# Kernel optimization log

Hardware: AMD Instinct MI355X
Metric: run time of the kernel (lower is better)

The kernel has to match this reference:

```python
import jax, jax.numpy as jnp
import numpy as np

N, T, F, T_dim, D = 256, 12, 32, 8, 64

def setup_inputs() -> dict:
    key = jax.random.key(0)
    ks = jax.random.split(key, 8)
    return {
        "x": jax.random.normal(ks[0], (N, T, F), jnp.float32),
        "Wq": jax.random.normal(ks[1], (N * T_dim, F, D), jnp.float32) * 0.1,
        "Wk": jax.random.normal(ks[2], (N * T_dim, F, D), jnp.float32) * 0.1,
        "Wv": jax.random.normal(ks[3], (N * T_dim, F, D), jnp.float32) * 0.1,
        "bq": jnp.zeros((N * T_dim, 1, D), jnp.float32),
        "bk": jnp.zeros((N * T_dim, 1, D), jnp.float32),
        "bv": jnp.zeros((N * T_dim, 1, D), jnp.float32),
        "w1": jax.random.normal(ks[4], (T_dim, T_dim * T * T), jnp.float32) * (2.0 / (T_dim * T * T)) ** 0.5,
        "b1": jnp.zeros((T_dim,), jnp.float32),
        "w2": jax.random.normal(ks[5], (1, T_dim), jnp.float32) * 0.5,
        "b2": jnp.zeros((1,), jnp.float32),
        "w3": jax.random.normal(ks[6], (D, D * T_dim), jnp.float32) * (2.0 / (D * T_dim)) ** 0.5,
        "b3": jnp.zeros((D,), jnp.float32),
        "w4": jax.random.normal(ks[7], (F, D), jnp.float32) * (2.0 / D) ** 0.5,
        "b4": jnp.zeros((F,), jnp.float32),
    }

def reference(x, Wq, Wk, Wv, bq, bk, bv, w1, b1, w2, b2, w3, b3, w4, b4):
    norm = 1.0 / np.sqrt(D).astype(np.float32)
    # mat_a: (N*T_dim, T, F) -- x broadcast across T_dim 'time scales'
    mat_a = jnp.broadcast_to(x[:, None], (N, T_dim, T, F)).reshape(-1, T, F)
    q = jnp.einsum('btf,bfd->btd', mat_a, Wq) + bq  # (N*T_dim, T, D)
    k = jnp.einsum('btf,bfd->btd', mat_a, Wk) + bk
    v = jnp.einsum('btf,bfd->btd', mat_a, Wv) + bv
    q4 = q.reshape(N, T_dim, T, D)
    k4 = k.reshape(N, T_dim, T, D)
    # pairwise scores: (N, N, T_dim, T, T)
    alpha = jnp.einsum('iktd,jksd->ijkts', q4, k4) * norm
    alpha = alpha.reshape(N, N, T_dim * T * T)
    h = jax.nn.relu(alpha @ w1.T + b1)            # (N, N, T_dim); dropout = identity (eval)
    s = (h @ w2.T + b2)[..., 0]                   # (N, N)
    att_score = jax.nn.softmax(s, axis=1)
    v4 = v.reshape(N, T_dim, T, D)
    b = jnp.einsum('ij,jktd->iktd', att_score, v4)   # (N, T_dim, T, D)
    b = b.transpose(0, 2, 3, 1).reshape(N, T, D * T_dim)
    y = jax.nn.relu(b @ w3.T + b3)                # (N, T, D); dropout = identity (eval)
    y = y @ w4.T + b4                             # (N, T, F)
    return (y, att_score)
```

## Files before the change

kernel.cpp:

```cpp
#include <hip/hip_runtime.h>
#include <hip/hip_bf16.h>

typedef unsigned short ushort_t;
typedef __bf16 bf16x8 __attribute__((ext_vector_type(8)));
typedef float f32x4 __attribute__((ext_vector_type(4)));
typedef ushort_t ushort8 __attribute__((ext_vector_type(8)));
typedef ushort_t ushort4v __attribute__((ext_vector_type(4)));

#define GLOAD16(gp, lp) \
    __builtin_amdgcn_global_load_lds((const __attribute__((address_space(1))) void*)(gp), \
                                     (__attribute__((address_space(3))) void*)(lp), 16, 0, 0)

__device__ __forceinline__ ushort_t bf16bits(float x) {
    __hip_bfloat16 h = __float2bfloat16(x);
    return *(ushort_t*)&h;
}
__device__ __forceinline__ float bf2f(ushort_t u) {
    unsigned v = (unsigned)u << 16;
    float f;
    __builtin_memcpy(&f, &v, 4);
    return f;
}

__global__ __launch_bounds__(256) void qkv_kernel(
    const float* __restrict__ x,
    const float* __restrict__ Wq, const float* __restrict__ Wk, const float* __restrict__ Wv,
    const float* __restrict__ bq, const float* __restrict__ bk, const float* __restrict__ bv,
    ushort_t* __restrict__ qhi, ushort_t* __restrict__ kbf, ushort_t* __restrict__ vbf)
{
    __shared__ float xs[4][12 * 36];
    int tid = threadIdx.x;
    int wid = tid >> 6, l = tid & 63;
    int gid = blockIdx.x * 4 + wid;
    int mat = gid >> 11, b = gid & 2047;
    int j = b >> 3;

    const float* W    = (mat == 0) ? Wq : (mat == 1) ? Wk : Wv;
    const float* bias = (mat == 0) ? bq : (mat == 1) ? bk : bv;
    ushort_t*    out  = (mat == 0) ? qhi : (mat == 1) ? kbf : vbf;
    float scale = (mat == 0) ? 0.125f : 1.0f;

    {
        const float4* xsrc = (const float4*)(x + (size_t)j * 384);
        float4 g0 = xsrc[l];
        int flat0 = l * 4;
        float* dst0 = &xs[wid][(flat0 >> 5) * 36 + (flat0 & 31)];
        dst0[0] = g0.x; dst0[1] = g0.y; dst0[2] = g0.z; dst0[3] = g0.w;
        if (l < 32) {
            float4 g1 = xsrc[64 + l];
            int flat1 = 256 + l * 4;
            float* dst1 = &xs[wid][(flat1 >> 5) * 36 + (flat1 & 31)];
            dst1[0] = g1.x; dst1[1] = g1.y; dst1[2] = g1.z; dst1[3] = g1.w;
        }
    }
    __syncthreads();

    int dq = l & 15, tg = l >> 4;
    const f32x4* w4 = (const f32x4*)(W + (size_t)b * 2048);
    f32x4 a0 = {0.f,0.f,0.f,0.f}, a1 = a0, a2 = a0;
    const float* xr = &xs[wid][tg * 3 * 36];
    #pragma unroll
    for (int f4 = 0; f4 < 8; ++f4) {
        f32x4 w0 = w4[(f4 * 4 + 0) * 16 + dq];
        f32x4 w1_ = w4[(f4 * 4 + 1) * 16 + dq];
        f32x4 w2_ = w4[(f4 * 4 + 2) * 16 + dq];
        f32x4 w3_ = w4[(f4 * 4 + 3) * 16 + dq];
        float4 xa = *(const float4*)&xr[0 * 36 + f4 * 4];
        float4 xb = *(const float4*)&xr[1 * 36 + f4 * 4];
        float4 xc = *(const float4*)&xr[2 * 36 + f4 * 4];
        a0 += w0 * xa.x + w1_ * xa.y + w2_ * xa.z + w3_ * xa.w;
        a1 += w0 * xb.x + w1_ * xb.y + w2_ * xb.z + w3_ * xb.w;
        a2 += w0 * xc.x + w1_ * xc.y + w2_ * xc.z + w3_ * xc.w;
    }

    f32x4 bv4 = *(const f32x4*)(bias + (size_t)b * 64 + dq * 4);
    size_t obase = (size_t)b * 768 + dq * 4;
    f32x4 r;
    ushort4v u;
    r = (a0 + bv4) * scale;
    u[0] = bf16bits(r[0]); u[1] = bf16bits(r[1]); u[2] = bf16bits(r[2]); u[3] = bf16bits(r[3]);
    *(ushort4v*)(out + obase + (size_t)(tg * 3 + 0) * 64) = u;
    r = (a1 + bv4) * scale;
    u[0] = bf16bits(r[0]); u[1] = bf16bits(r[1]); u[2] = bf16bits(r[2]); u[3] = bf16bits(r[3]);
    *(ushort4v*)(out + obase + (size_t)(tg * 3 + 1) * 64) = u;
    r = (a2 + bv4) * scale;
    u[0] = bf16bits(r[0]); u[1] = bf16bits(r[1]); u[2] = bf16bits(r[2]); u[3] = bf16bits(r[3]);
    *(ushort4v*)(out + obase + (size_t)(tg * 3 + 2) * 64) = u;
}

__global__ __launch_bounds__(256) void gbuild_kernel(
    const ushort_t* __restrict__ kbf, const float* __restrict__ w1,
    const ushort_t* __restrict__ vbf, const float* __restrict__ w3, const float* __restrict__ w4,
    ushort_t* __restrict__ ghi, ushort_t* __restrict__ vt,
    float* __restrict__ w3t, float* __restrict__ w4t)
{
    __shared__ alignas(16) char sbuf[8448];
    int bx = blockIdx.x, tid = threadIdx.x;

    if (bx < 2048) {
        float* w1s = (float*)sbuf;
        float* ks  = (float*)sbuf + 1152;
        int b = bx, j = b >> 3, kk = b & 7;

        #pragma unroll
        for (int r = 0; r < 2; ++r) {
            int c = r * 256 + tid;
            if (c < 288)
                GLOAD16(w1 + (c / 36) * 1152 + kk * 144 + (c % 36) * 4, &w1s[c * 4]);
        }
        if (tid < 96) {
            ushort8 uu = *(const ushort8*)(kbf + (size_t)b * 768 + tid * 8);
            float4 f0, f1;
            f0.x = bf2f(uu[0]); f0.y = bf2f(uu[1]); f0.z = bf2f(uu[2]); f0.w = bf2f(uu[3]);
            f1.x = bf2f(uu[4]); f1.y = bf2f(uu[5]); f1.z = bf2f(uu[6]); f1.w = bf2f(uu[7]);
            ((float4*)ks)[tid * 2]     = f0;
            ((float4*)ks)[tid * 2 + 1] = f1;
        }
        __syncthreads();

        #pragma unroll
        for (int r = 0; r < 3; ++r) {
            int e = r * 256 + tid;
            int m = e / 96, rem = e - m * 96;
            int t = rem >> 3, d8 = rem & 7;
            const float* w1p = w1s + m * 144 + t * 12;
            float acc[8] = {0.f,0.f,0.f,0.f,0.f,0.f,0.f,0.f};
            #pragma unroll
            for (int s = 0; s < 12; ++s) {
                float wv = w1p[s];
                const float4* kp = (const float4*)(ks + s * 64 + d8 * 8);
                float4 k0 = kp[0], k1 = kp[1];
                acc[0] += wv * k0.x; acc[1] += wv * k0.y;
                acc[2] += wv * k0.z; acc[3] += wv * k0.w;
                acc[4] += wv * k1.x; acc[5] += wv * k1.y;
                acc[6] += wv * k1.z; acc[7] += wv * k1.w;
            }
            ushort8 u;
            #pragma unroll
            for (int dd = 0; dd < 8; ++dd) u[dd] = bf16bits(acc[dd]);
            *(ushort8*)(ghi + ((size_t)j * 8 + m) * 6144 + kk * 768 + t * 64 + d8 * 8) = u;
        }
        return;
    }

    if (bx < 2432) {
        ushort_t (*ts)[264] = (ushort_t(*)[264])sbuf;
        int c0 = (bx - 2048) * 16;
        int cc = tid & 15, jg = tid >> 4;
        #pragma unroll 4
        for (int jj = 0; jj < 16; ++jj) {
            int jx = jg * 16 + jj;
            ts[cc][jx] = vbf[(size_t)jx * 6144 + c0 + cc];
        }
        __syncthreads();
        #pragma unroll
        for (int c = 0; c < 16; ++c)
            vt[(size_t)(c0 + c) * 256 + tid] = ts[c][tid];
        return;
    }
    if (bx < 2448) {
        int wb = bx - 2432;
        #pragma unroll
        for (int r = 0; r < 8; ++r) {
            int e = wb * 2048 + r * 256 + tid;
            int dout = e >> 9, c3 = e & 511;
            int cb = ((c3 & 7) << 6) | (c3 >> 3);
            w3t[cb * 64 + dout] = w3[e];
        }
        return;
    }
    #pragma unroll
    for (int r = 0; r < 8; ++r) {
        int e = r * 256 + tid; int f = e >> 6, dd = e & 63;
        w4t[dd * 32 + f] = w4[e];
    }
}

__global__ __launch_bounds__(256, 2) void hgemm_kernel(
    const ushort_t* __restrict__ qhi, const ushort_t* __restrict__ ghi,
    ushort_t* __restrict__ hpart)
{
    __shared__ ushort_t As[2][128 * 64];
    __shared__ ushort_t Bs[2][128 * 64];

    int tid = threadIdx.x;
    int bid = blockIdx.x;
    int lane = tid & 63, wid = tid >> 6;
    int wr = wid >> 1, wc = wid & 1;
    int xcd = bid & 7, kq = bid >> 3;
    int z = xcd + 8 * (kq >> 5);
    int rem = kq & 31;
    int n0 = (rem & 15) * 128, i0 = (rem >> 4) * 128;
    int kbase = z * 384;
    ushort_t* Hout = hpart + (size_t)z * 524288;

    f32x4 acc[4][4] = {};

    #define STAGE(buf, koff)                                                                 \
    {                                                                                        \
        _Pragma("unroll")                                                                    \
        for (int r = 0; r < 4; ++r) {                                                        \
            int c = r * 256 + tid; int row = c >> 3, slot = c & 7;                           \
            int so = (koff) + ((slot ^ (row & 7)) * 8);                                      \
            GLOAD16(ghi + (size_t)(n0 + row) * 6144 + so, &As[buf][c * 8]);                  \
            GLOAD16(qhi + (size_t)(i0 + row) * 6144 + so, &Bs[buf][c * 8]);                  \
        }                                                                                    \
    }

    STAGE(0, kbase);
    int cur = 0;
    for (int s = 0; s < 6; ++s) {
        __syncthreads();
        if (s + 1 < 6) STAGE(cur ^ 1, kbase + (s + 1) * 64);
        #pragma unroll
        for (int kh = 0; kh < 2; ++kh) {
            bf16x8 a[4], b[4];
            #pragma unroll
            for (int mi = 0; mi < 4; ++mi) {
                int row = wr * 64 + mi * 16 + (lane & 15);
                int slot = (kh * 4 + (lane >> 4)) ^ (row & 7);
                a[mi] = *(const bf16x8*)&As[cur][row * 64 + slot * 8];
            }
            #pragma unroll
            for (int ni = 0; ni < 4; ++ni) {
                int row = wc * 64 + ni * 16 + (lane & 15);
                int slot = (kh * 4 + (lane >> 4)) ^ (row & 7);
                b[ni] = *(const bf16x8*)&Bs[cur][row * 64 + slot * 8];
            }
            #pragma unroll
            for (int mi = 0; mi < 4; ++mi)
                #pragma unroll
                for (int ni = 0; ni < 4; ++ni)
                    acc[mi][ni] = __builtin_amdgcn_mfma_f32_16x16x32_bf16(a[mi], b[ni], acc[mi][ni], 0, 0, 0);
        }
        cur ^= 1;
    }
    #undef STAGE

    int r4 = (lane >> 4) * 4, cn = lane & 15;
    #pragma unroll
    for (int mi = 0; mi < 4; ++mi)
        #pragma unroll
        for (int ni = 0; ni < 4; ++ni) {
            int i = i0 + wc * 64 + ni * 16 + cn;
            int nb = n0 + wr * 64 + mi * 16 + r4;
            ushort4v u;
            #pragma unroll
            for (int r = 0; r < 4; ++r) u[r] = bf16bits(acc[mi][ni][r]);
            *(ushort4v*)(Hout + (size_t)i * 2048 + nb) = u;
        }
}

__global__ __launch_bounds__(256) void score_softmax_kernel(
    const ushort_t* __restrict__ hpart, const float* __restrict__ b1g,
    const float* __restrict__ w2g, const float* __restrict__ b2g,
    float* __restrict__ att, ushort_t* __restrict__ attbf)
{
    int i = blockIdx.x, j = threadIdx.x;
    float hm[8];
    #pragma unroll
    for (int m = 0; m < 8; ++m) hm[m] = b1g[m];
    #pragma unroll 4
    for (int z = 0; z < 16; ++z) {
        ushort8 u = *(const ushort8*)(hpart + (size_t)z * 524288 + (size_t)i * 2048 + j * 8);
        #pragma unroll
        for (int m = 0; m < 8; ++m) hm[m] += bf2f(u[m]);
    }
    float sv = b2g[0];
    #pragma unroll
    for (int m = 0; m < 8; ++m) sv += fmaxf(hm[m], 0.f) * w2g[m];

    __shared__ float wred[4], wred2[4];
    float mx = sv;
    #pragma unroll
    for (int off = 32; off > 0; off >>= 1) mx = fmaxf(mx, __shfl_down(mx, off, 64));
    if ((j & 63) == 0) wred[j >> 6] = mx;
    __syncthreads();
    mx = fmaxf(fmaxf(wred[0], wred[1]), fmaxf(wred[2], wred[3]));

    float e = expf(sv - mx);
    float sum = e;
    #pragma unroll
    for (int off = 32; off > 0; off >>= 1) sum += __shfl_down(sum, off, 64);
    if ((j & 63) == 0) wred2[j >> 6] = sum;
    __syncthreads();
    sum = wred2[0] + wred2[1] + wred2[2] + wred2[3];

    float pv = e / sum;
    att[(size_t)i * 256 + j] = pv;
    attbf[(size_t)i * 256 + j] = bf16bits(pv);
}

__global__ __launch_bounds__(256) void av_kernel(
    const ushort_t* __restrict__ attbf, const ushort_t* __restrict__ vt,
    float* __restrict__ bmat)
{
    __shared__ ushort_t As[2][64 * 64];
    __shared__ ushort_t Bs[2][64 * 64];

    int tid = threadIdx.x, lane = tid & 63, wid = tid >> 6;
    int wr = wid >> 1, wc = wid & 1;
    int c0 = blockIdx.x * 64, i0 = blockIdx.y * 64;

    f32x4 acc[2][2] = {};

    #define STAGEAV(buf, koff)                                                              \
    {                                                                                       \
        _Pragma("unroll")                                                                   \
        for (int r = 0; r < 2; ++r) {                                                       \
            int c = r * 256 + tid; int row = c >> 3, slot = c & 7;                          \
            int so = (koff) + ((slot ^ (row & 7)) * 8);                                     \
            GLOAD16(vt + (size_t)(c0 + row) * 256 + so, &As[buf][c * 8]);                   \
            GLOAD16(attbf + (size_t)(i0 + row) * 256 + so, &Bs[buf][c * 8]);                \
        }                                                                                   \
    }

    int cur = 0;
    STAGEAV(0, 0);
    for (int s = 0; s < 4; ++s) {
        __syncthreads();
        if (s < 3) STAGEAV(cur ^ 1, (s + 1) * 64);
        #pragma unroll
        for (int kh = 0; kh < 2; ++kh) {
            bf16x8 a[2], b[2];
            #pragma unroll
            for (int mi = 0; mi < 2; ++mi) {
                int row = wr * 32 + mi * 16 + (lane & 15);
                int slot = (kh * 4 + (lane >> 4)) ^ (row & 7);
                a[mi] = *(const bf16x8*)&As[cur][row * 64 + slot * 8];
            }
            #pragma unroll
            for (int ni = 0; ni < 2; ++ni) {
                int row = wc * 32 + ni * 16 + (lane & 15);
                int slot = (kh * 4 + (lane >> 4)) ^ (row & 7);
                b[ni] = *(const bf16x8*)&Bs[cur][row * 64 + slot * 8];
            }
            #pragma unroll
            for (int mi = 0; mi < 2; ++mi)
                #pragma unroll
                for (int ni = 0; ni < 2; ++ni)
                    acc[mi][ni] = __builtin_amdgcn_mfma_f32_16x16x32_bf16(a[mi], b[ni], acc[mi][ni], 0, 0, 0);
        }
        cur ^= 1;
    }
    #undef STAGEAV

    int r4 = (lane >> 4) * 4, cn = lane & 15;
    #pragma unroll
    for (int mi = 0; mi < 2; ++mi)
        #pragma unroll
        for (int ni = 0; ni < 2; ++ni) {
            int i = i0 + wc * 32 + ni * 16 + cn;
            int c = c0 + wr * 32 + mi * 16 + r4;
            int kk = c / 768, rem = c - kk * 768;
            int t = rem >> 6, d = rem & 63;
            float4 val;
            val.x = acc[mi][ni][0]; val.y = acc[mi][ni][1];
            val.z = acc[mi][ni][2]; val.w = acc[mi][ni][3];
            *(float4*)(bmat + ((size_t)i * 12 + t) * 512 + kk * 64 + d) = val;
        }
}

__global__ __launch_bounds__(256) void out_kernel(
    const float* __restrict__ bmat, const float* __restrict__ w3t, const float* __restrict__ b3,
    const float* __restrict__ w4t, const float* __restrict__ b4, float* __restrict__ yout)
{
    int rb = blockIdx.x * 8;
    int tid = threadIdx.x;
    __shared__ float rows[8 * 512];
    __shared__ float y1s[8 * 64];
    const float4* src = (const float4*)(bmat + (size_t)rb * 512);
    #pragma unroll
    for (int r = 0; r < 4; ++r) ((float4*)rows)[tid + r * 256] = src[tid + r * 256];
    __syncthreads();

    int dout = tid & 63, rg = tid >> 6;
    float acc[2];
    float b3v = b3[dout];
    acc[0] = b3v; acc[1] = b3v;
    for (int c4 = 0; c4 < 128; ++c4) {
        float w0 = w3t[(c4 * 4 + 0) * 64 + dout];
        float w1v = w3t[(c4 * 4 + 1) * 64 + dout];
        float w2v = w3t[(c4 * 4 + 2) * 64 + dout];
        float w3v = w3t[(c4 * 4 + 3) * 64 + dout];
        #pragma unroll
        for (int jj = 0; jj < 2; ++jj) {
            float4 rv = *(const float4*)&rows[(rg * 2 + jj) * 512 + c4 * 4];
            acc[jj] += rv.x * w0 + rv.y * w1v + rv.z * w2v + rv.w * w3v;
        }
    }
    #pragma unroll
    for (int jj = 0; jj < 2; ++jj) y1s[(rg * 2 + jj) * 64 + dout] = fmaxf(acc[jj], 0.f);
    __syncthreads();

    int f = tid & 31, rh = tid >> 5;
    float a2 = b4[f];
    #pragma unroll
    for (int dd = 0; dd < 64; ++dd) a2 += y1s[rh * 64 + dd] * w4t[dd * 32 + f];
    yout[(size_t)(rb + rh) * 32 + f] = a2;
}

extern "C" void kernel_launch(void* const* d_in, const int* in_sizes, int n_in,
                              void* d_out, int out_size, void* d_ws, size_t ws_size,
                              hipStream_t stream) {
    (void)in_sizes; (void)n_in; (void)out_size; (void)ws_size;
    const float* x  = (const float*)d_in[0];
    const float* Wq = (const float*)d_in[1];
    const float* Wk = (const float*)d_in[2];
    const float* Wv = (const float*)d_in[3];
    const float* bq = (const float*)d_in[4];
    const float* bk = (const float*)d_in[5];
    const float* bv = (const float*)d_in[6];
    const float* w1 = (const float*)d_in[7];
    const float* b1 = (const float*)d_in[8];
    const float* w2 = (const float*)d_in[9];
    const float* b2 = (const float*)d_in[10];
    const float* w3 = (const float*)d_in[11];
    const float* b3 = (const float*)d_in[12];
    const float* w4 = (const float*)d_in[13];
    const float* b4 = (const float*)d_in[14];

    float* ws = (float*)d_ws;
    ushort_t* hpart = (ushort_t*)ws;
    size_t    off   = 4194304;
    ushort_t* qhi   = (ushort_t*)(ws + off);
    ushort_t* ghi   = (ushort_t*)(ws + off + 786432);
    ushort_t* vbf   = (ushort_t*)(ws + off + 7077888);
    ushort_t* vt    = (ushort_t*)(ws + off + 7864320);
    ushort_t* attbf = (ushort_t*)(ws + off + 8650752);
    float*    w3t   = ws + off + 8683520;
    float*    w4t   = ws + off + 8716288;
    ushort_t* kbf   = (ushort_t*)(ws + off + 8718336);
    float*    bmat  = (float*)ghi;

    float* yout = (float*)d_out;
    float* att  = (float*)d_out + 98304;

    qkv_kernel<<<1536, 256, 0, stream>>>(x, Wq, Wk, Wv, bq, bk, bv, qhi, kbf, vbf);
    gbuild_kernel<<<2449, 256, 0, stream>>>(kbf, w1, vbf, w3, w4, ghi, vt, w3t, w4t);
    hgemm_kernel<<<512, 256, 0, stream>>>(qhi, ghi, hpart);
    score_softmax_kernel<<<256, 256, 0, stream>>>(hpart, b1, w2, b2, att, attbf);
    av_kernel<<<dim3(96, 4), 256, 0, stream>>>(attbf, vt, bmat);
    out_kernel<<<384, 256, 0, stream>>>(bmat, w3t, b3, w4t, b4, yout);
}
```

Baseline: 75.42 us.

## Fuse G-matrix construction into hgemm and merge auxiliary transposes into its launch

Removes the separate gbuild kernel. Each hgemm block now computes its 64-row slice of the w1·k product in registers and writes it straight into LDS as the A tile, instead of reading a precomputed ghi matrix from global memory. Block tiling changes to 64 A rows by the full 256 Q rows, with the whole Q tile streamed through a larger shared buffer. The v transpose and the w3/w4 transposes ride along as extra blocks in the same launch. This saves a launch and the ghi global round-trip, at the cost of a larger LDS footprint (~77KB, likely limiting occupancy), redundant G computation across blocks, and extra VALU work interleaved with the MFMA loop.

```diff
diff --git a/kernel.cpp b/kernel.cpp
--- a/kernel.cpp
+++ b/kernel.cpp
@@ -88,162 +88,159 @@
     *(ushort4v*)(out + obase + (size_t)(tg * 3 + 2) * 64) = u;
 }
 
-__global__ __launch_bounds__(256) void gbuild_kernel(
-    const ushort_t* __restrict__ kbf, const float* __restrict__ w1,
+__global__ __launch_bounds__(256, 2) void hgemm_kernel(
+    const ushort_t* __restrict__ qhi, const ushort_t* __restrict__ kbf,
+    const float* __restrict__ w1, ushort_t* __restrict__ hpart,
     const ushort_t* __restrict__ vbf, const float* __restrict__ w3, const float* __restrict__ w4,
-    ushort_t* __restrict__ ghi, ushort_t* __restrict__ vt,
-    float* __restrict__ w3t, float* __restrict__ w4t)
+    ushort_t* __restrict__ vt, float* __restrict__ w3t, float* __restrict__ w4t)
 {
-    __shared__ alignas(16) char sbuf[8448];
-    int bx = blockIdx.x, tid = threadIdx.x;
-
-    if (bx < 2048) {
-        float* w1s = (float*)sbuf;
-        float* ks  = (float*)sbuf + 1152;
-        int b = bx, j = b >> 3, kk = b & 7;
-
-        #pragma unroll
-        for (int r = 0; r < 2; ++r) {
-            int c = r * 256 + tid;
-            if (c < 288)
-                GLOAD16(w1 + (c / 36) * 1152 + kk * 144 + (c % 36) * 4, &w1s[c * 4]);
-        }
-        if (tid < 96) {
-            ushort8 uu = *(const ushort8*)(kbf + (size_t)b * 768 + tid * 8);
-            float4 f0, f1;
-            f0.x = bf2f(uu[0]); f0.y = bf2f(uu[1]); f0.z = bf2f(uu[2]); f0.w = bf2f(uu[3]);
-            f1.x = bf2f(uu[4]); f1.y = bf2f(uu[5]); f1.z = bf2f(uu[6]); f1.w = bf2f(uu[7]);
-            ((float4*)ks)[tid * 2]     = f0;
-            ((float4*)ks)[tid * 2 + 1] = f1;
-        }
-        __syncthreads();
-
-        #pragma unroll
-        for (int r = 0; r < 3; ++r) {
-            int e = r * 256 + tid;
-            int m = e / 96, rem = e - m * 96;
-            int t = rem >> 3, d8 = rem & 7;
-            const float* w1p = w1s + m * 144 + t * 12;
-            float acc[8] = {0.f,0.f,0.f,0.f,0.f,0.f,0.f,0.f};
-            #pragma unroll
-            for (int s = 0; s < 12; ++s) {
-                float wv = w1p[s];
-                const float4* kp = (const float4*)(ks + s * 64 + d8 * 8);
-                float4 k0 = kp[0], k1 = kp[1];
-                acc[0] += wv * k0.x; acc[1] += wv * k0.y;
-                acc[2] += wv * k0.z; acc[3] += wv * k0.w;
-                acc[4] += wv * k1.x; acc[5] += wv * k1.y;
-                acc[6] += wv * k1.z; acc[7] += wv * k1.w;
-            }
-            ushort8 u;
-            #pragma unroll
-            for (int dd = 0; dd < 8; ++dd) u[dd] = bf16bits(acc[dd]);
-            *(ushort8*)(ghi + ((size_t)j * 8 + m) * 6144 + kk * 768 + t * 64 + d8 * 8) = u;
-        }
-        return;
-    }
-
-    if (bx < 2432) {
-        ushort_t (*ts)[264] = (ushort_t(*)[264])sbuf;
-        int c0 = (bx - 2048) * 16;
-        int cc = tid & 15, jg = tid >> 4;
-        #pragma unroll 4
-        for (int jj = 0; jj < 16; ++jj) {
-            int jx = jg * 16 + jj;
-            ts[cc][jx] = vbf[(size_t)jx * 6144 + c0 + cc];
-        }
-        __syncthreads();
-        #pragma unroll
-        for (int c = 0; c < 16; ++c)
-            vt[(size_t)(c0 + c) * 256 + tid] = ts[c][tid];
-        return;
-    }
-    if (bx < 2448) {
-        int wb = bx - 2432;
-        #pragma unroll
-        for (int r = 0; r < 8; ++r) {
-            int e = wb * 2048 + r * 256 + tid;
-            int dout = e >> 9, c3 = e & 511;
-            int cb = ((c3 & 7) << 6) | (c3 >> 3);
-            w3t[cb * 64 + dout] = w3[e];
-        }
-        return;
-    }
-    #pragma unroll
-    for (int r = 0; r < 8; ++r) {
-        int e = r * 256 + tid; int f = e >> 6, dd = e & 63;
-        w4t[dd * 32 + f] = w4[e];
-    }
-}
-
-__global__ __launch_bounds__(256, 2) void hgemm_kernel(
-    const ushort_t* __restrict__ qhi, const ushort_t* __restrict__ ghi,
-    ushort_t* __restrict__ hpart)
-{
-    __shared__ ushort_t As[2][128 * 64];
-    __shared__ ushort_t Bs[2][128 * 64];
-
+    __shared__ alignas(16) char sb[77056];
     int tid = threadIdx.x;
     int bid = blockIdx.x;
-    int lane = tid & 63, wid = tid >> 6;
-    int wr = wid >> 1, wc = wid & 1;
+
+    if (bid >= 512) {
+        if (bid < 896) {
+            ushort_t (*ts)[264] = (ushort_t(*)[264])sb;
+            int c0 = (bid - 512) * 16;
+            int cc = tid & 15, jg = tid >> 4;
+            #pragma unroll 4
+            for (int jj = 0; jj < 16; ++jj) {
+                int jx = jg * 16 + jj;
+                ts[cc][jx] = vbf[(size_t)jx * 6144 + c0 + cc];
+            }
+            __syncthreads();
+            #pragma unroll
+            for (int c = 0; c < 16; ++c)
+                vt[(size_t)(c0 + c) * 256 + tid] = ts[c][tid];
+            return;
+        }
+        if (bid < 912) {
+            int wb = bid - 896;
+            #pragma unroll
+            for (int r = 0; r < 8; ++r) {
+                int e = wb * 2048 + r * 256 + tid;
+                int dout = e >> 9, c3 = e & 511;
+                int cb = ((c3 & 7) << 6) | (c3 >> 3);
+                w3t[cb * 64 + dout] = w3[e];
+            }
+            return;
+        }
+        #pragma unroll
+        for (int r = 0; r < 8; ++r) {
+            int e = r * 256 + tid; int f = e >> 6, dd = e & 63;
+            w4t[dd * 32 + f] = w4[e];
+        }
+        return;
+    }
+
+    ushort_t* Bs  = (ushort_t*)sb;
+    ushort_t* As  = (ushort_t*)(sb + 65536);
+    float*    w1s = (float*)(sb + 74752);
+
+    int lane = tid & 63, wv = tid >> 6;
     int xcd = bid & 7, kq = bid >> 3;
     int z = xcd + 8 * (kq >> 5);
     int rem = kq & 31;
-    int n0 = (rem & 15) * 128, i0 = (rem >> 4) * 128;
-    int kbase = z * 384;
+    int n0 = rem * 64, jb = rem * 8;
+    int kk = z >> 1, thalf = (z & 1) * 6;
     ushort_t* Hout = hpart + (size_t)z * 524288;
 
+    int j_loc = tid >> 5, d8 = (tid >> 2) & 7, mg = tid & 3;
+
+    if (tid < 144) {
+        int m = tid / 18, r = tid % 18;
+        GLOAD16(w1 + (size_t)m * 1152 + kk * 144 + thalf * 12 + r * 4, &w1s[m * 72 + r * 4]);
+    }
+    ushort8 kreg[12];
+    {
+        const ushort_t* kp = kbf + (size_t)((jb + j_loc) * 8 + kk) * 768 + d8 * 8;
+        #pragma unroll
+        for (int s = 0; s < 12; ++s) kreg[s] = *(const ushort8*)(kp + s * 64);
+    }
+    __syncthreads();
+
     f32x4 acc[4][4] = {};
 
-    #define STAGE(buf, koff)                                                                 \
-    {                                                                                        \
-        _Pragma("unroll")                                                                    \
-        for (int r = 0; r < 4; ++r) {                                                        \
-            int c = r * 256 + tid; int row = c >> 3, slot = c & 7;                           \
-            int so = (koff) + ((slot ^ (row & 7)) * 8);                                      \
-            GLOAD16(ghi + (size_t)(n0 + row) * 6144 + so, &As[buf][c * 8]);                  \
-            GLOAD16(qhi + (size_t)(i0 + row) * 6144 + so, &Bs[buf][c * 8]);                  \
-        }                                                                                    \
-    }
-
-    STAGE(0, kbase);
+    #define GBUILD(st)                                                          \
+    {                                                                           \
+        float ag0[8] = {0.f,0.f,0.f,0.f,0.f,0.f,0.f,0.f};                       \
+        float ag1[8] = {0.f,0.f,0.f,0.f,0.f,0.f,0.f,0.f};                       \
+        _Pragma("unroll")                                                       \
+        for (int s = 0; s < 12; ++s) {                                          \
+            float kf[8];                                                        \
+            _Pragma("unroll")                                                   \
+            for (int dd = 0; dd < 8; ++dd) kf[dd] = bf2f(kreg[s][dd]);          \
+            float wa = w1s[(mg * 2 + 0) * 72 + (st) * 12 + s];                  \
+            float wb = w1s[(mg * 2 + 1) * 72 + (st) * 12 + s];                  \
+            _Pragma("unroll")                                                   \
+            for (int dd = 0; dd < 8; ++dd) {                                    \
+                ag0[dd] += wa * kf[dd];                                         \
+                ag1[dd] += wb * kf[dd];                                         \
+            }                                                                   \
+        }                                                                       \
+        int row0 = j_loc * 8 + mg * 2;                                          \
+        int sl0 = d8 ^ (row0 & 7), sl1 = d8 ^ ((row0 + 1) & 7);                 \
+        ushort8 u0, u1;                                                         \
+        _Pragma("unroll")                                                       \
+        for (int dd = 0; dd < 8; ++dd) { u0[dd] = bf16bits(ag0[dd]); u1[dd] = bf16bits(ag1[dd]); } \
+        *(ushort8*)&As[row0 * 72 + sl0 * 8] = u0;                               \
+        *(ushort8*)&As[(row0 + 1) * 72 + sl1 * 8] = u1;                         \
+    }
+
+    #define STAGE_B(buf, st)                                                    \
+    {                                                                           \
+        int koff = kk * 768 + (thalf + (st)) * 64;                              \
+        _Pragma("unroll")                                                       \
+        for (int r = 0; r < 8; ++r) {                                           \
+            int c = r * 256 + tid; int row = c >> 3, slot = c & 7;              \
+            GLOAD16(qhi + (size_t)row * 6144 + koff + ((slot ^ (row & 7)) * 8), \
+                    &Bs[(buf) * 16384 + c * 8]);                                \
+        }                                                                       \
+    }
+
+    GBUILD(0);
+    STAGE_B(0, 0);
     int cur = 0;
-    for (int s = 0; s < 6; ++s) {
+    for (int st = 0; st < 6; ++st) {
         __syncthreads();
-        if (s + 1 < 6) STAGE(cur ^ 1, kbase + (s + 1) * 64);
-        #pragma unroll
-        for (int kh = 0; kh < 2; ++kh) {
-            bf16x8 a[4], b[4];
+        bf16x8 a[2][4], b[2][4];
+        #pragma unroll
+        for (int kh = 0; kh < 2; ++kh)
             #pragma unroll
             for (int mi = 0; mi < 4; ++mi) {
-                int row = wr * 64 + mi * 16 + (lane & 15);
+                int row = mi * 16 + (lane & 15);
                 int slot = (kh * 4 + (lane >> 4)) ^ (row & 7);
-                a[mi] = *(const bf16x8*)&As[cur][row * 64 + slot * 8];
-            }
+                a[kh][mi] = *(const bf16x8*)&As[row * 72 + slot * 8];
+            }
+        #pragma unroll
+        for (int kh = 0; kh < 2; ++kh)
             #pragma unroll
             for (int ni = 0; ni < 4; ++ni) {
-                int row = wc * 64 + ni * 16 + (lane & 15);
+                int row = wv * 64 + ni * 16 + (lane & 15);
                 int slot = (kh * 4 + (lane >> 4)) ^ (row & 7);
-                b[ni] = *(const bf16x8*)&Bs[cur][row * 64 + slot * 8];
-            }
+                b[kh][ni] = *(const bf16x8*)&Bs[cur * 16384 + row * 64 + slot * 8];
+            }
+        __syncthreads();
+        if (st + 1 < 6) { GBUILD(st + 1); STAGE_B(cur ^ 1, st + 1); }
+        #pragma unroll
+        for (int kh = 0; kh < 2; ++kh)
             #pragma unroll
             for (int mi = 0; mi < 4; ++mi)
                 #pragma unroll
                 for (int ni = 0; ni < 4; ++ni)
-                    acc[mi][ni] = __builtin_amdgcn_mfma_f32_16x16x32_bf16(a[mi], b[ni], acc[mi][ni], 0, 0, 0);
-        }
+                    acc[mi][ni] = __builtin_amdgcn_mfma_f32_16x16x32_bf16(a[kh][mi], b[kh][ni], acc[mi][ni], 0, 0, 0);
         cur ^= 1;
     }
-    #undef STAGE
+    #undef GBUILD
+    #undef STAGE_B
 
     int r4 = (lane >> 4) * 4, cn = lane & 15;
     #pragma unroll
     for (int mi = 0; mi < 4; ++mi)
         #pragma unroll
         for (int ni = 0; ni < 4; ++ni) {
-            int i = i0 + wc * 64 + ni * 16 + cn;
-            int nb = n0 + wr * 64 + mi * 16 + r4;
+            int i = wv * 64 + ni * 16 + cn;
+            int nb = n0 + mi * 16 + r4;
             ushort4v u;
             #pragma unroll
             for (int r = 0; r < 4; ++r) u[r] = bf16bits(acc[mi][ni][r]);
@@ -424,21 +421,19 @@
     ushort_t* hpart = (ushort_t*)ws;
     size_t    off   = 4194304;
     ushort_t* qhi   = (ushort_t*)(ws + off);
-    ushort_t* ghi   = (ushort_t*)(ws + off + 786432);
-    ushort_t* vbf   = (ushort_t*)(ws + off + 7077888);
-    ushort_t* vt    = (ushort_t*)(ws + off + 7864320);
-    ushort_t* attbf = (ushort_t*)(ws + off + 8650752);
-    float*    w3t   = ws + off + 8683520;
-    float*    w4t   = ws + off + 8716288;
-    ushort_t* kbf   = (ushort_t*)(ws + off + 8718336);
-    float*    bmat  = (float*)ghi;
+    ushort_t* kbf   = (ushort_t*)(ws + off + 786432);
+    ushort_t* vbf   = (ushort_t*)(ws + off + 1572864);
+    ushort_t* vt    = (ushort_t*)(ws + off + 2359296);
+    ushort_t* attbf = (ushort_t*)(ws + off + 3145728);
+    float*    w3t   = ws + off + 3178496;
+    float*    w4t   = ws + off + 3211264;
+    float*    bmat  = ws + off + 3213312;
 
     float* yout = (float*)d_out;
     float* att  = (float*)d_out + 98304;
 
     qkv_kernel<<<1536, 256, 0, stream>>>(x, Wq, Wk, Wv, bq, bk, bv, qhi, kbf, vbf);
-    gbuild_kernel<<<2449, 256, 0, stream>>>(kbf, w1, vbf, w3, w4, ghi, vt, w3t, w4t);
-    hgemm_kernel<<<512, 256, 0, stream>>>(qhi, ghi, hpart);
+    hgemm_kernel<<<913, 256, 0, stream>>>(qhi, kbf, w1, hpart, vbf, w3, w4, vt, w3t, w4t);
     score_softmax_kernel<<<256, 256, 0, stream>>>(hpart, b1, w2, b2, att, attbf);
     av_kernel<<<dim3(96, 4), 256, 0, stream>>>(attbf, vt, bmat);
     out_kernel<<<384, 256, 0, stream>>>(bmat, w3t, b3, w4t, b4, yout);
```

Result: faster. 62.11 us (median of 3 runs) (-17.6%).
